# Kernel tuning notes

Hardware: AMD Instinct MI355X
Metric: run time of the kernel (lower is better)

## Reference

```python
import jax, jax.numpy as jnp
import numpy as np

EPS = 1e-10
COMMITMENT_COST = 0.25


def setup_inputs() -> dict:
    key = jax.random.key(0)
    k1, k2 = jax.random.split(key)
    inputs = jax.random.normal(k1, (64, 64, 32, 32), dtype=jnp.float32)
    # nn.init.uniform_(weight, -1.0, 1.0)
    embeddings = jax.random.uniform(k2, (1024, 64), dtype=jnp.float32, minval=-1.0, maxval=1.0)
    return {"inputs": inputs, "embeddings": embeddings}


def reference(inputs, embeddings):
    B, C, H, W = inputs.shape  # C == embedding_dim
    K = embeddings.shape[0]
    x = jnp.transpose(inputs, (0, 2, 3, 1)).reshape(-1, C)  # [N, D]
    d = (jnp.sum(x * x, axis=1, keepdims=True)
         - 2.0 * (x @ embeddings.T)
         + jnp.sum(embeddings * embeddings, axis=1))  # [N, K]
    idx = jnp.argmin(d, axis=1)  # [N]
    # one-hot @ embeddings == gather
    q = jnp.take(embeddings, idx, axis=0)  # [N, D]
    x4 = x.reshape(B, H, W, C)
    q4 = q.reshape(B, H, W, C)
    e_latent = jnp.mean((jax.lax.stop_gradient(q4) - x4) ** 2)
    q_latent = jnp.mean((q4 - jax.lax.stop_gradient(x4)) ** 2)
    loss = q_latent + COMMITMENT_COST * e_latent
    # straight-through estimator
    st = x4 + jax.lax.stop_gradient(q4 - x4)
    # avg_probs = mean of one-hot encodings == normalized histogram
    n = idx.shape[0]
    avg_probs = jnp.zeros((K,), dtype=jnp.float32).at[idx].add(1.0) / n
    perplexity = jnp.exp(-jnp.sum(avg_probs * jnp.log(avg_probs + EPS)))
    quantized = jnp.transpose(st, (0, 3, 1, 2))
    return quantized, loss, perplexity
```

## Files before the change

kernel.cpp:

```cpp
#include <hip/hip_runtime.h>

#define N_TOTAL   65536
#define HW_SZ     1024
#define CDIM      64
#define K_CODES   1024
#define OUT_ELEMS 4194304
#define QT        256
#define NCHUNK    4
#define TAU       0.004f


typedef __attribute__((ext_vector_type(8))) short short8;
typedef __attribute__((ext_vector_type(4))) float f32x4;

__device__ __forceinline__ unsigned short f2bf(float x) {
    unsigned u = __float_as_uint(x);
    return (unsigned short)((u + 0x7FFFu + ((u >> 16) & 1u)) >> 16);
}
__device__ __forceinline__ float bf2f(unsigned short h) {
    return __uint_as_float(((unsigned)h) << 16);
}
__device__ __forceinline__ void gload_lds16(const void* g, void* l) {
    __builtin_amdgcn_global_load_lds(
        (const __attribute__((address_space(1))) void*)g,
        (__attribute__((address_space(3))) void*)l, 16, 0, 0);
}

__global__ void k_prep(const float* __restrict__ emb, float* __restrict__ enorm,
                       short* __restrict__ btab, unsigned int* __restrict__ hist) {
    int gid = blockIdx.x * 256 + threadIdx.x;
    int r  = gid >> 4;
    int d0 = (gid & 15) * 4;
    float4 v = *(const float4*)(emb + gid * 4);
    float s = v.x * v.x + v.y * v.y + v.z * v.z + v.w * v.w;
#pragma unroll
    for (int off = 1; off < 16; off <<= 1) s += __shfl_xor(s, off, 64);
    if ((gid & 15) == 0) enorm[r] = s;

    float vv[4] = {v.x, v.y, v.z, v.w};
    short h[4], l[4];
#pragma unroll
    for (int j = 0; j < 4; ++j) {
        unsigned short hh = f2bf(vv[j]);
        h[j] = (short)hh;
        l[j] = (short)f2bf(vv[j] - bf2f(hh));
    }
    int base = (r >> 4) * 2048 + (d0 >> 5) * 1024
             + ((((d0 >> 3) & 3) * 16 + (r & 15)) * 8) + (d0 & 7);
    *(short4*)&btab[base]       = make_short4(h[0], h[1], h[2], h[3]);
    *(short4*)&btab[base + 512] = make_short4(l[0], l[1], l[2], l[3]);

    if (gid < K_CODES) hist[gid] = 0u;
}

__global__ __launch_bounds__(512, 2)
void k_argmin(const float* __restrict__ x, const float* __restrict__ emb,
              const short* __restrict__ btab, const float* __restrict__ enorm,
              unsigned int* __restrict__ hist, float* __restrict__ partials,
              float* __restrict__ out) {
    __shared__ __align__(16) short bufs[2][16 * 2048];
    __shared__ __align__(16) float ens[K_CODES];
    __shared__ float xnorm[QT];
    __shared__ float rd1[QT];
    __shared__ float rd2[QT];
    __shared__ int   ri[QT];
    __shared__ int   flist[QT];
    __shared__ __align__(16) float xqf[CDIM];
    __shared__ float wdd[8];
    __shared__ int   wii[8];
    __shared__ float spw[4];
    __shared__ int   nflag;
    float* tile = (float*)bufs;

    const int tid  = threadIdx.x;
    const int lane = tid & 63;
    const int w    = tid >> 6;
    const int quad = lane >> 4;
    const int col  = lane & 15;

    const int n0  = blockIdx.x * QT;
    const int b   = n0 >> 10;
    const int hw0 = n0 & 1023;

    auto stage_async = [&](int c, int bsel) {
        const short* src = btab + c * (16 * 2048);
#pragma unroll
        for (int i = 0; i < 8; ++i) {
            int idx = i * 512 + tid;
            gload_lds16(&src[idx * 8], (void*)&bufs[bsel][idx * 8]);
        }
    };

    stage_async(0, 0);
    if (tid < 256) gload_lds16(&enorm[tid * 4], (void*)&ens[tid * 4]);

    const float* xb = x + b * (CDIM * HW_SZ) + hw0 + col;
    short8 afr[2][2][2];
#pragma unroll
    for (int rt = 0; rt < 2; ++rt) {
        float nloc = 0.f;
#pragma unroll
        for (int kc = 0; kc < 2; ++kc) {
#pragma unroll
            for (int j = 0; j < 8; ++j) {
                int c0 = (kc * 4 + quad) * 8 + j;
                float v = xb[c0 * HW_SZ + w * 32 + rt * 16];
                unsigned short hh = f2bf(v);
                afr[rt][kc][0][j] = (short)hh;
                afr[rt][kc][1][j] = (short)f2bf(v - bf2f(hh));
                nloc = __builtin_fmaf(v, v, nloc);
            }
        }
        nloc += __shfl_xor(nloc, 16, 64);
        nloc += __shfl_xor(nloc, 32, 64);
        if (quad == 0) xnorm[w * 32 + rt * 16 + col] = nloc;
    }

    float d1[8], d2[8];
    int   i1[8];
#pragma unroll
    for (int t = 0; t < 8; ++t) { d1[t] = 3.4e38f; d2[t] = 3.4e38f; i1[t] = 0; }

    __syncthreads();

    for (int c = 0; c < NCHUNK; ++c) {
        if (c + 1 < NCHUNK) stage_async(c + 1, (c + 1) & 1);
        const short* bs = &bufs[c & 1][0];
        const int cbase = c * 256;

        short8 Ba[4], Bb[4];
        float  ena, enb;
        auto LDB = [&](short8 (&B)[4], float& en, int ctl) {
            const short* fp = bs + ctl * 2048 + lane * 8;
            B[0] = *(const short8*)(fp);
            B[1] = *(const short8*)(fp + 512);
            B[2] = *(const short8*)(fp + 1024);
            B[3] = *(const short8*)(fp + 1536);
            en   = ens[cbase + ctl * 16 + col];
        };
        auto COMP = [&](const short8 (&B)[4], float en, int mycode) {
#pragma unroll
            for (int rt = 0; rt < 2; ++rt) {
                f32x4 a0 = {0.f, 0.f, 0.f, 0.f};
                f32x4 a1 = {0.f, 0.f, 0.f, 0.f};
                a0 = __builtin_amdgcn_mfma_f32_16x16x32_bf16(afr[rt][0][1], B[0], a0, 0, 0, 0);
                a1 = __builtin_amdgcn_mfma_f32_16x16x32_bf16(afr[rt][1][1], B[2], a1, 0, 0, 0);
                a0 = __builtin_amdgcn_mfma_f32_16x16x32_bf16(afr[rt][0][0], B[1], a0, 0, 0, 0);
                a1 = __builtin_amdgcn_mfma_f32_16x16x32_bf16(afr[rt][1][0], B[3], a1, 0, 0, 0);
                a0 = __builtin_amdgcn_mfma_f32_16x16x32_bf16(afr[rt][0][0], B[0], a0, 0, 0, 0);
                a1 = __builtin_amdgcn_mfma_f32_16x16x32_bf16(afr[rt][1][0], B[2], a1, 0, 0, 0);
#pragma unroll
                for (int reg = 0; reg < 4; ++reg) {
                    int t = rt * 4 + reg;
                    float dot = a0[reg] + a1[reg];
                    float d   = __builtin_fmaf(dot, -2.f, en);
                    float d1o = d1[t];
                    d2[t] = __builtin_amdgcn_fmed3f(d, d1o, d2[t]);
                    d1[t] = fminf(d, d1o);
                    i1[t] = (d < d1o) ? mycode : i1[t];
                }
            }
        };

        LDB(Ba, ena, 0);
#pragma unroll
        for (int ctl = 0; ctl < 16; ctl += 2) {
            LDB(Bb, enb, ctl + 1);
            COMP(Ba, ena, cbase + ctl * 16 + col);
            if (ctl + 2 < 16) LDB(Ba, ena, ctl + 2);
            COMP(Bb, enb, cbase + (ctl + 1) * 16 + col);
        }
        __syncthreads();
    }

#pragma unroll
    for (int t = 0; t < 8; ++t) {
        float a1 = d1[t], a2 = d2[t];
        int ai = i1[t];
#pragma unroll
        for (int off = 1; off < 16; off <<= 1) {
            float o1 = __shfl_xor(a1, off, 64);
            float o2 = __shfl_xor(a2, off, 64);
            int   oi = __shfl_xor(ai, off, 64);
            if (o1 < a1 || (o1 == a1 && oi < ai)) {
                float loser = a1; a2 = fminf(fminf(a2, o2), loser); a1 = o1; ai = oi;
            } else {
                a2 = fminf(fminf(a2, o2), o1);
            }
        }
        d1[t] = a1; d2[t] = a2; i1[t] = ai;
    }

    if (tid == 0) nflag = 0;
    if (col == 0) {
#pragma unroll
        for (int rt = 0; rt < 2; ++rt)
#pragma unroll
            for (int reg = 0; reg < 4; ++reg) {
                int t = rt * 4 + reg;
                int m = w * 32 + rt * 16 + quad * 4 + reg;
                rd1[m] = d1[t];
                rd2[m] = d2[t];
                ri [m] = i1[t];
            }
    }
    __syncthreads();

    if (tid < QT) {
        if (rd2[tid] - rd1[tid] < TAU) {
            int slot = atomicAdd(&nflag, 1);
            flist[slot] = tid;
        }
    }
    __syncthreads();

    for (int f = 0; f < nflag; ++f) {
        const int q = flist[f];
        if (tid < CDIM) xqf[tid] = x[b * (CDIM * HW_SZ) + tid * HW_SZ + hw0 + q];
        __syncthreads();
        float dm = 3.4e38f; int im = 0;
#pragma unroll
        for (int cd = 0; cd < 2; ++cd) {
            const int k = tid + cd * 512;
            const float4* er = (const float4*)(emb + k * CDIM);
            const float4* xr = (const float4*)xqf;
            float dot = 0.f;
#pragma unroll
            for (int c4 = 0; c4 < 16; ++c4) {
                float4 e = er[c4], xv = xr[c4];
                dot += e.x * xv.x + e.y * xv.y + e.z * xv.z + e.w * xv.w;
            }
            float d = ens[k] - 2.f * dot;
            if (d < dm) { dm = d; im = k; }
        }
#pragma unroll
        for (int off = 1; off < 64; off <<= 1) {
            float od = __shfl_xor(dm, off, 64);
            int   oi = __shfl_xor(im, off, 64);
            if (od < dm || (od == dm && oi < im)) { dm = od; im = oi; }
        }
        if (lane == 0) { wdd[w] = dm; wii[w] = im; }
        __syncthreads();
        if (tid == 0) {
            float bd = wdd[0]; int bi = wii[0];
#pragma unroll
            for (int ww = 1; ww < 8; ++ww)
                if (wdd[ww] < bd || (wdd[ww] == bd && wii[ww] < bi)) { bd = wdd[ww]; bi = wii[ww]; }
            rd1[q] = bd; ri[q] = bi;
        }
        __syncthreads();
    }

    if (tid < QT) {
        int ai = ri[tid];
        atomicAdd(&hist[ai], 1u);
        float sp = rd1[tid] + xnorm[tid];
#pragma unroll
        for (int off = 32; off; off >>= 1) sp += __shfl_down(sp, off, 64);
        if (lane == 0) spw[w] = sp;
    }
    __syncthreads();
    if (tid == 0) partials[blockIdx.x] = spw[0] + spw[1] + spw[2] + spw[3];

#pragma unroll
    for (int h = 0; h < 4; ++h) {
        {
            int q = tid >> 3, j8 = tid & 7;
            int code = ri[h * 64 + q];
            int ct = code >> 4, cl = code & 15;
            int kc = j8 >> 2, qd = j8 & 3;
            const short* tb = btab + ct * 2048 + kc * 1024;
            short8 hi = *(const short8*)&tb[(qd * 16 + cl) * 8];
            short8 lo = *(const short8*)&tb[512 + (qd * 16 + cl) * 8];
            float* dst = &tile[q * 72 + j8 * 8];
#pragma unroll
            for (int k = 0; k < 8; ++k)
                dst[k] = bf2f((unsigned short)hi[k]) + bf2f((unsigned short)lo[k]);
        }
        __syncthreads();
        {
            int c = tid >> 3;
            float* ob = out + b * (CDIM * HW_SZ) + c * HW_SZ + hw0 + h * 64;
#pragma unroll
            for (int p = 0; p < 2; ++p) {
                int q = ((tid & 7) + p * 8) * 4;
                float4 v;
                v.x = tile[(q + 0) * 72 + c];
                v.y = tile[(q + 1) * 72 + c];
                v.z = tile[(q + 2) * 72 + c];
                v.w = tile[(q + 3) * 72 + c];
                *(float4*)&ob[q] = v;
            }
        }
        if (h < 3) __syncthreads();
    }
}

__global__ void k_final(const float* __restrict__ partials,
                        const unsigned int* __restrict__ hist,
                        float* __restrict__ out) {
    int tid = threadIdx.x;
    float ss = partials[tid];
    float s = 0.f;
#pragma unroll
    for (int i = 0; i < 4; ++i) {
        float p = (float)hist[i * 256 + tid] * (1.0f / 65536.0f);
        s += p * logf(p + 1e-10f);
    }
    __shared__ float fin[8];
#pragma unroll
    for (int off = 32; off; off >>= 1) {
        ss += __shfl_down(ss, off, 64);
        s  += __shfl_down(s, off, 64);
    }
    if ((tid & 63) == 0) { fin[tid >> 6] = ss; fin[4 + (tid >> 6)] = s; }
    __syncthreads();
    if (tid == 0) {
        float sse = fin[0] + fin[1] + fin[2] + fin[3];
        float ent = fin[4] + fin[5] + fin[6] + fin[7];
        out[OUT_ELEMS]     = 1.25f * sse * (1.0f / (float)OUT_ELEMS);
        out[OUT_ELEMS + 1] = expf(-ent);
    }
}

extern "C" void kernel_launch(void* const* d_in, const int* in_sizes, int n_in,
                              void* d_out, int out_size, void* d_ws, size_t ws_size,
                              hipStream_t stream) {
    const float* x   = (const float*)d_in[0];
    const float* emb = (const float*)d_in[1];
    float* out = (float*)d_out;
    char* ws = (char*)d_ws;
    float*        enorm    = (float*)(ws);
    unsigned int* hist     = (unsigned int*)(ws + 4096);
    float*        partials = (float*)(ws + 8192);
    short*        btab     = (short*)(ws + 12288);

    k_prep  <<<64, 256, 0, stream>>>(emb, enorm, btab, hist);
    k_argmin<<<N_TOTAL / QT, 512, 0, stream>>>(x, emb, btab, enorm, hist, partials, out);
    k_final <<<1, 256, 0, stream>>>(partials, hist, out);
}
```

Before: 124.2 us.

## Replace global histogram atomics with per-block LDS histograms reduced in final kernel

Each argmin block now builds its histogram in shared memory with LDS atomics and writes a packed 16-bit-pair copy of all 1024 bins to a per-block workspace slot, rather than issuing global atomicAdds. The final kernel, now run with 1024 threads, sums the 256 per-block histograms before computing entropy. This removes contended global atomics and the histogram zeroing in the prep kernel. In exchange each block writes 2KB of extra global data and the single-block final kernel must read about 512KB serially, which may cost more than the atomics did.

```diff
diff --git a/kernel.cpp b/kernel.cpp
--- a/kernel.cpp
+++ b/kernel.cpp
@@ -7,6 +7,7 @@
 #define OUT_ELEMS 4194304
 #define QT        256
 #define NCHUNK    4
+#define NBLK      (N_TOTAL / QT)
 #define TAU       0.004f
 
 
@@ -27,7 +28,7 @@
 }
 
 __global__ void k_prep(const float* __restrict__ emb, float* __restrict__ enorm,
-                       short* __restrict__ btab, unsigned int* __restrict__ hist) {
+                       short* __restrict__ btab) {
     int gid = blockIdx.x * 256 + threadIdx.x;
     int r  = gid >> 4;
     int d0 = (gid & 15) * 4;
@@ -49,14 +50,12 @@
              + ((((d0 >> 3) & 3) * 16 + (r & 15)) * 8) + (d0 & 7);
     *(short4*)&btab[base]       = make_short4(h[0], h[1], h[2], h[3]);
     *(short4*)&btab[base + 512] = make_short4(l[0], l[1], l[2], l[3]);
-
-    if (gid < K_CODES) hist[gid] = 0u;
 }
 
 __global__ __launch_bounds__(512, 2)
 void k_argmin(const float* __restrict__ x, const float* __restrict__ emb,
               const short* __restrict__ btab, const float* __restrict__ enorm,
-              unsigned int* __restrict__ hist, float* __restrict__ partials,
+              unsigned int* __restrict__ hbuf, float* __restrict__ partials,
               float* __restrict__ out) {
     __shared__ __align__(16) short bufs[2][16 * 2048];
     __shared__ __align__(16) float ens[K_CODES];
@@ -71,6 +70,7 @@
     __shared__ float spw[4];
     __shared__ int   nflag;
     float* tile = (float*)bufs;
+    unsigned int* lhist = (unsigned int*)((char*)bufs + 32768);
 
     const int tid  = threadIdx.x;
     const int lane = tid & 63;
@@ -251,15 +251,17 @@
         __syncthreads();
     }
 
+    lhist[tid] = 0u; lhist[512 + tid] = 0u;
+    __syncthreads();
+    if (tid < QT) atomicAdd(&lhist[ri[tid]], 1u);
     if (tid < QT) {
-        int ai = ri[tid];
-        atomicAdd(&hist[ai], 1u);
         float sp = rd1[tid] + xnorm[tid];
 #pragma unroll
         for (int off = 32; off; off >>= 1) sp += __shfl_down(sp, off, 64);
-        if (lane == 0) spw[w] = sp;
-    }
-    __syncthreads();
+        if (lane == 0) spw[tid >> 6] = sp;
+    }
+    __syncthreads();
+    hbuf[blockIdx.x * 512 + tid] = lhist[2 * tid] | (lhist[2 * tid + 1] << 16);
     if (tid == 0) partials[blockIdx.x] = spw[0] + spw[1] + spw[2] + spw[3];
 
 #pragma unroll
@@ -296,28 +298,45 @@
     }
 }
 
-__global__ void k_final(const float* __restrict__ partials,
-                        const unsigned int* __restrict__ hist,
-                        float* __restrict__ out) {
-    int tid = threadIdx.x;
-    float ss = partials[tid];
-    float s = 0.f;
-#pragma unroll
-    for (int i = 0; i < 4; ++i) {
-        float p = (float)hist[i * 256 + tid] * (1.0f / 65536.0f);
-        s += p * logf(p + 1e-10f);
-    }
-    __shared__ float fin[8];
+__global__ __launch_bounds__(1024, 1)
+void k_final(const unsigned int* __restrict__ hbuf,
+             const float* __restrict__ partials, float* __restrict__ out) {
+    __shared__ unsigned int hc[2][512][2];
+    __shared__ float fin[32];
+    const int tid  = threadIdx.x;
+    const int tlo  = tid & 511;
+    const int half = tid >> 9;
+
+    unsigned c0 = 0, c1 = 0;
+#pragma unroll 8
+    for (int r = 0; r < NBLK / 2; ++r) {
+        unsigned v = hbuf[(half * (NBLK / 2) + r) * 512 + tlo];
+        c0 += v & 0xffffu;
+        c1 += v >> 16;
+    }
+    hc[half][tlo][0] = c0;
+    hc[half][tlo][1] = c1;
+    __syncthreads();
+
+    float s = 0.f, ss = 0.f;
+    if (half == 0) {
+        float p0 = (float)(hc[0][tlo][0] + hc[1][tlo][0]) * (1.0f / 65536.0f);
+        float p1 = (float)(hc[0][tlo][1] + hc[1][tlo][1]) * (1.0f / 65536.0f);
+        s = p0 * logf(p0 + 1e-10f) + p1 * logf(p1 + 1e-10f);
+        if (tlo < NBLK) ss = partials[tlo];
+    }
 #pragma unroll
     for (int off = 32; off; off >>= 1) {
         ss += __shfl_down(ss, off, 64);
         s  += __shfl_down(s, off, 64);
     }
-    if ((tid & 63) == 0) { fin[tid >> 6] = ss; fin[4 + (tid >> 6)] = s; }
+    const int w = tid >> 6;
+    if ((tid & 63) == 0) { fin[w] = ss; fin[16 + w] = s; }
     __syncthreads();
     if (tid == 0) {
-        float sse = fin[0] + fin[1] + fin[2] + fin[3];
-        float ent = fin[4] + fin[5] + fin[6] + fin[7];
+        float sse = 0.f, ent = 0.f;
+#pragma unroll
+        for (int i = 0; i < 16; ++i) { sse += fin[i]; ent += fin[16 + i]; }
         out[OUT_ELEMS]     = 1.25f * sse * (1.0f / (float)OUT_ELEMS);
         out[OUT_ELEMS + 1] = expf(-ent);
     }
@@ -331,11 +350,11 @@
     float* out = (float*)d_out;
     char* ws = (char*)d_ws;
     float*        enorm    = (float*)(ws);
-    unsigned int* hist     = (unsigned int*)(ws + 4096);
     float*        partials = (float*)(ws + 8192);
     short*        btab     = (short*)(ws + 12288);
-
-    k_prep  <<<64, 256, 0, stream>>>(emb, enorm, btab, hist);
-    k_argmin<<<N_TOTAL / QT, 512, 0, stream>>>(x, emb, btab, enorm, hist, partials, out);
-    k_final <<<1, 256, 0, stream>>>(partials, hist, out);
-}
+    unsigned int* hbuf     = (unsigned int*)(ws + 274432);
+
+    k_prep  <<<64, 256, 0, stream>>>(emb, enorm, btab);
+    k_argmin<<<NBLK, 512, 0, stream>>>(x, emb, btab, enorm, hbuf, partials, out);
+    k_final <<<1, 1024, 0, stream>>>(hbuf, partials, out);
+}
```

Result: slower. 127.2 us (+2.4%).

## Use per-wave exact rescoring and direct fp32 gather for quantized output

Applied to the files above, without the earlier changes.

The exact-distance fallback for near-tie queries now assigns one flagged query to each wave, and each wave scans all codes on its own. This removes the two block-wide barriers and the cross-wave reduction that every flagged query used to pay. The output write no longer rebuilds values from the split bf16 table and transposes them through shared memory. It gathers fp32 embedding values directly from global memory and writes float4 rows, dropping several barriers. The cost is uncoalesced scattered reads of emb, which the L2 cache should absorb since the table is 256KB.

```diff
diff --git a/kernel.cpp b/kernel.cpp
--- a/kernel.cpp
+++ b/kernel.cpp
@@ -65,12 +65,9 @@
     __shared__ float rd2[QT];
     __shared__ int   ri[QT];
     __shared__ int   flist[QT];
-    __shared__ __align__(16) float xqf[CDIM];
-    __shared__ float wdd[8];
-    __shared__ int   wii[8];
+    __shared__ __align__(16) float xqfw[8][64];
     __shared__ float spw[4];
     __shared__ int   nflag;
-    float* tile = (float*)bufs;
 
     const int tid  = threadIdx.x;
     const int lane = tid & 63;
@@ -214,20 +211,18 @@
     }
     __syncthreads();
 
-    for (int f = 0; f < nflag; ++f) {
+    for (int f = w; f < nflag; f += 8) {
         const int q = flist[f];
-        if (tid < CDIM) xqf[tid] = x[b * (CDIM * HW_SZ) + tid * HW_SZ + hw0 + q];
-        __syncthreads();
+        xqfw[w][lane] = x[b * (CDIM * HW_SZ) + lane * HW_SZ + hw0 + q];
         float dm = 3.4e38f; int im = 0;
-#pragma unroll
-        for (int cd = 0; cd < 2; ++cd) {
-            const int k = tid + cd * 512;
+        for (int cd = 0; cd < 16; ++cd) {
+            const int k = cd * 64 + lane;
             const float4* er = (const float4*)(emb + k * CDIM);
-            const float4* xr = (const float4*)xqf;
             float dot = 0.f;
 #pragma unroll
             for (int c4 = 0; c4 < 16; ++c4) {
-                float4 e = er[c4], xv = xr[c4];
+                float4 e  = er[c4];
+                float4 xv = *(const float4*)&xqfw[w][c4 * 4];
                 dot += e.x * xv.x + e.y * xv.y + e.z * xv.z + e.w * xv.w;
             }
             float d = ens[k] - 2.f * dot;
@@ -239,17 +234,9 @@
             int   oi = __shfl_xor(im, off, 64);
             if (od < dm || (od == dm && oi < im)) { dm = od; im = oi; }
         }
-        if (lane == 0) { wdd[w] = dm; wii[w] = im; }
-        __syncthreads();
-        if (tid == 0) {
-            float bd = wdd[0]; int bi = wii[0];
-#pragma unroll
-            for (int ww = 1; ww < 8; ++ww)
-                if (wdd[ww] < bd || (wdd[ww] == bd && wii[ww] < bi)) { bd = wdd[ww]; bi = wii[ww]; }
-            rd1[q] = bd; ri[q] = bi;
-        }
-        __syncthreads();
-    }
+        if (lane == 0) { rd1[q] = dm; ri[q] = im; }
+    }
+    __syncthreads();
 
     if (tid < QT) {
         int ai = ri[tid];
@@ -257,42 +244,25 @@
         float sp = rd1[tid] + xnorm[tid];
 #pragma unroll
         for (int off = 32; off; off >>= 1) sp += __shfl_down(sp, off, 64);
-        if (lane == 0) spw[w] = sp;
+        if (lane == 0) spw[tid >> 6] = sp;
     }
     __syncthreads();
     if (tid == 0) partials[blockIdx.x] = spw[0] + spw[1] + spw[2] + spw[3];
 
-#pragma unroll
-    for (int h = 0; h < 4; ++h) {
-        {
-            int q = tid >> 3, j8 = tid & 7;
-            int code = ri[h * 64 + q];
-            int ct = code >> 4, cl = code & 15;
-            int kc = j8 >> 2, qd = j8 & 3;
-            const short* tb = btab + ct * 2048 + kc * 1024;
-            short8 hi = *(const short8*)&tb[(qd * 16 + cl) * 8];
-            short8 lo = *(const short8*)&tb[512 + (qd * 16 + cl) * 8];
-            float* dst = &tile[q * 72 + j8 * 8];
-#pragma unroll
-            for (int k = 0; k < 8; ++k)
-                dst[k] = bf2f((unsigned short)hi[k]) + bf2f((unsigned short)lo[k]);
-        }
-        __syncthreads();
-        {
-            int c = tid >> 3;
-            float* ob = out + b * (CDIM * HW_SZ) + c * HW_SZ + hw0 + h * 64;
-#pragma unroll
-            for (int p = 0; p < 2; ++p) {
-                int q = ((tid & 7) + p * 8) * 4;
-                float4 v;
-                v.x = tile[(q + 0) * 72 + c];
-                v.y = tile[(q + 1) * 72 + c];
-                v.z = tile[(q + 2) * 72 + c];
-                v.w = tile[(q + 3) * 72 + c];
-                *(float4*)&ob[q] = v;
-            }
-        }
-        if (h < 3) __syncthreads();
+    {
+        const int q0 = lane * 4;
+        const int c0 = ri[q0], c1 = ri[q0 + 1], c2 = ri[q0 + 2], c3 = ri[q0 + 3];
+        float* ob = out + b * (CDIM * HW_SZ) + hw0 + q0;
+#pragma unroll
+        for (int cc = 0; cc < 8; ++cc) {
+            const int c = w * 8 + cc;
+            float4 v;
+            v.x = emb[c0 * CDIM + c];
+            v.y = emb[c1 * CDIM + c];
+            v.z = emb[c2 * CDIM + c];
+            v.w = emb[c3 * CDIM + c];
+            *(float4*)&ob[c * HW_SZ] = v;
+        }
     }
 }
 
```

New measurement: 134.1 us. 8.0% more time.
